# Kernel optimization log

Hardware: AMD Instinct MI355X
Metric: run time of the kernel (lower is better)

The kernel has to match this reference:

```python
import jax, jax.numpy as jnp
import numpy as np

B, S, H, L = 4096, 64, 768, 5
TEMP = 0.07
BN_EPS = 1e-5


def setup_inputs() -> dict:
    key = jax.random.key(0)
    ks = jax.random.split(key, 8)
    seq = jax.random.normal(ks[0], (B, S, H), dtype=jnp.float32)
    labels = jax.random.randint(ks[1], (B,), 0, L)
    s = 1.0 / np.sqrt(H)
    return {
        'sequence_output': seq,
        'cls_gamma': jnp.ones((H,), jnp.float32),
        'cls_beta': jnp.zeros((H,), jnp.float32),
        'cls_W': jax.random.normal(ks[2], (H, H), jnp.float32) * s,
        'cls_b': jax.random.normal(ks[3], (H,), jnp.float32) * 0.01,
        'label_gamma': jnp.ones((H,), jnp.float32),
        'label_beta': jnp.zeros((H,), jnp.float32),
        'label_W': jax.random.normal(ks[4], (H, H), jnp.float32) * s,
        'label_b': jax.random.normal(ks[5], (H,), jnp.float32) * 0.01,
        'labels': labels,
    }


def _batchnorm(x, gamma, beta):
    # training-mode BatchNorm1d: biased batch stats
    m = x.mean(0)
    v = jnp.mean((x - m) ** 2, axis=0)
    return (x - m) * jax.lax.rsqrt(v + BN_EPS) * gamma + beta


def _l2norm(x):
    return x / jnp.sqrt(jnp.sum(x * x, axis=-1, keepdims=True)).clip(1e-12)


def reference(sequence_output, cls_gamma, cls_beta, cls_W, cls_b,
              label_gamma, label_beta, label_W, label_b, labels):
    z = sequence_output[:, 0, :]  # [B,H]; dropout is identity in eval
    # label token spans: 'No relation' -> positions 1:3 (mean), rest single tokens 3..6
    theta = jnp.stack([
        sequence_output[:, 1:3, :].mean(axis=1),
        sequence_output[:, 3, :],
        sequence_output[:, 4, :],
        sequence_output[:, 5, :],
        sequence_output[:, 6, :],
    ], axis=1)  # [B,L,H]
    z_cl, theta_cl = z, theta

    zp = _batchnorm(z, cls_gamma, cls_beta) @ cls_W.T + cls_b  # [B,H]
    tp = _batchnorm(theta.reshape(-1, H), label_gamma, label_beta) @ label_W.T + label_b
    tp = tp.reshape(-1, L, H)  # [B,L,H]
    logits = jnp.einsum('blh,bh->bl', tp, zp)  # [B,L]

    # ---- dual supervised contrastive loss (vectorized over the python loops) ----
    z_norm = _l2norm(z_cl)        # [B,H]
    theta_norm = _l2norm(theta_cl)  # [B,L,H]
    same = labels[:, None] == labels[None, :]          # [B,B]
    eye = jnp.eye(labels.shape[0], dtype=bool)
    pos_mask = (same & ~eye).astype(jnp.float32)       # positives (same label, j != i)
    neg_mask = (~same).astype(jnp.float32)             # negatives (different label)
    has_pos = (same & ~eye).any(axis=1)

    # l_z: anchor z_i vs theta_j[labels_i] (pos) and all theta_j[:] for diff-label j (neg)
    expS = jnp.exp(jnp.einsum('ih,jlh->ijl', z_norm, theta_norm) / TEMP)  # [B,B,L]
    expS_at_lab = jnp.take_along_axis(
        expS, jnp.broadcast_to(labels[:, None, None], expS.shape[:2] + (1,)), axis=2
    )[..., 0]  # expS[i,j,labels[i]] -> [B,B]
    pos_z = jnp.sum(expS_at_lab * pos_mask, axis=1)
    neg_z = jnp.sum(expS.sum(axis=-1) * neg_mask, axis=1)
    l_z = jnp.where(has_pos, -jnp.log(pos_z / (pos_z + neg_z + 1e-8)), 0.0).sum()

    # l_theta: anchor theta_i[labels_i] vs z_j
    anchor_theta = jnp.take_along_axis(theta_norm, labels[:, None, None], axis=1)[:, 0, :]  # [B,H]
    expT = jnp.exp(anchor_theta @ z_norm.T / TEMP)  # [B,B]
    pos_t = jnp.sum(expT * pos_mask, axis=1)
    neg_t = jnp.sum(expT * neg_mask, axis=1)
    l_t = jnp.where(has_pos, -jnp.log(pos_t / (pos_t + neg_t + 1e-8)), 0.0).sum()

    dual_loss = (l_z + l_t) / labels.shape[0]
    return logits, dual_loss
```

## Files before the change

kernel.cpp:

```cpp
#include <hip/hip_runtime.h>
#include <hip/hip_bf16.h>
#include <cstdint>
#include <cstddef>

#define B_N 4096
#define S_N 64
#define H_N 768
#define L_N 5
#define TEMP_INV (1.0f / 0.07f)
#define BN_EPS 1e-5f

typedef __attribute__((ext_vector_type(8))) short short8;
typedef __attribute__((ext_vector_type(4))) float f32x4;

__device__ __forceinline__ void async_copy16(void* lds, const void* g) {
  __builtin_amdgcn_global_load_lds(
      (const __attribute__((address_space(1))) unsigned int*)g,
      (__attribute__((address_space(3))) unsigned int*)lds, 16, 0, 0);
}

__device__ __forceinline__ unsigned short bf16b(float x) {
  __hip_bfloat16 h = __float2bfloat16(x);
  return *reinterpret_cast<unsigned short*>(&h);
}
__device__ __forceinline__ void store_bf16x4(void* p, float4 v) {
  ushort4 o = make_ushort4(bf16b(v.x), bf16b(v.y), bf16b(v.z), bf16b(v.w));
  *reinterpret_cast<ushort4*>(p) = o;
}

__device__ inline float block_reduce_sum256(float v, float* sbuf) {
#pragma unroll
  for (int off = 32; off > 0; off >>= 1) v += __shfl_down(v, off, 64);
  int lane = threadIdx.x & 63;
  int wid = threadIdx.x >> 6;
  __syncthreads();
  if (lane == 0) sbuf[wid] = v;
  __syncthreads();
  float r = 0.f;
  if (threadIdx.x == 0) r = sbuf[0] + sbuf[1] + sbuf[2] + sbuf[3];
  return r;
}

__global__ __launch_bounds__(256) void extract_kernel(
    const float* __restrict__ seq, __hip_bfloat16* __restrict__ zb,
    __hip_bfloat16* __restrict__ tb, float* __restrict__ zn_inv,
    float* __restrict__ thn_inv, float* __restrict__ sum_z,
    float* __restrict__ ssq_z, float* __restrict__ sum_t,
    float* __restrict__ ssq_t) {
  __shared__ float pr[8][6][3];
  int t = threadIdx.x;
  int wv = t >> 6, ln = t & 63;
  bool act = t < 192;
  int c4 = t * 4;
  int b0 = blockIdx.x * 8;
  float zs[4] = {}, zq[4] = {}, ts4[4] = {}, tq4[4] = {};
  for (int r = 0; r < 8; ++r) {
    int b = b0 + r;
    const float* base = seq + (size_t)b * (S_N * H_N);
    float pv[6] = {0.f, 0.f, 0.f, 0.f, 0.f, 0.f};
    if (act) {
      float4 z4 = *(const float4*)(base + c4);
      store_bf16x4(zb + (size_t)b * H_N + c4, z4);
      pv[0] = z4.x * z4.x + z4.y * z4.y + z4.z * z4.z + z4.w * z4.w;
      zs[0] += z4.x; zs[1] += z4.y; zs[2] += z4.z; zs[3] += z4.w;
      zq[0] += z4.x * z4.x; zq[1] += z4.y * z4.y;
      zq[2] += z4.z * z4.z; zq[3] += z4.w * z4.w;
#pragma unroll
      for (int l = 0; l < L_N; ++l) {
        float4 v4;
        if (l == 0) {
          float4 a4 = *(const float4*)(base + H_N + c4);
          float4 b4 = *(const float4*)(base + 2 * H_N + c4);
          v4 = make_float4(0.5f * (a4.x + b4.x), 0.5f * (a4.y + b4.y),
                           0.5f * (a4.z + b4.z), 0.5f * (a4.w + b4.w));
        } else {
          v4 = *(const float4*)(base + (size_t)(l + 2) * H_N + c4);
        }
        store_bf16x4(tb + ((size_t)b * L_N + l) * H_N + c4, v4);
        pv[1 + l] = v4.x * v4.x + v4.y * v4.y + v4.z * v4.z + v4.w * v4.w;
        ts4[0] += v4.x; ts4[1] += v4.y; ts4[2] += v4.z; ts4[3] += v4.w;
        tq4[0] += v4.x * v4.x; tq4[1] += v4.y * v4.y;
        tq4[2] += v4.z * v4.z; tq4[3] += v4.w * v4.w;
      }
    }
#pragma unroll
    for (int v = 0; v < 6; ++v) {
      float x = pv[v];
#pragma unroll
      for (int off = 32; off > 0; off >>= 1) x += __shfl_down(x, off, 64);
      if (ln == 0 && wv < 3) pr[r][v][wv] = x;
    }
  }
  __syncthreads();
  if (t < 48) {
    int r = t / 6, v = t - r * 6;
    float s = pr[r][v][0] + pr[r][v][1] + pr[r][v][2];
    float inv = 1.f / fmaxf(sqrtf(s), 1e-12f);
    int b = b0 + r;
    if (v == 0) zn_inv[b] = inv;
    else thn_inv[b * L_N + (v - 1)] = inv;
  }
  if (act) {
#pragma unroll
    for (int j = 0; j < 4; ++j) {
      atomicAdd(&sum_z[c4 + j], zs[j]);
      atomicAdd(&ssq_z[c4 + j], zq[j]);
      atomicAdd(&sum_t[c4 + j], ts4[j]);
      atomicAdd(&ssq_t[c4 + j], tq4[j]);
    }
  }
}

__global__ void count_kernel(const int* __restrict__ labels, int* __restrict__ cnt) {
  int i = blockIdx.x * 256 + threadIdx.x;
  if (i < B_N) atomicAdd(&cnt[labels[i]], 1);
}

__global__ void finalize_kernel(
    const float* __restrict__ sum_z, const float* __restrict__ ssq_z,
    const float* __restrict__ sum_t, const float* __restrict__ ssq_t,
    const float* __restrict__ g_z, const float* __restrict__ b_z,
    const float* __restrict__ g_t, const float* __restrict__ b_t,
    float* __restrict__ sz_s, float* __restrict__ sz_t,
    float* __restrict__ st_s, float* __restrict__ st_t) {
  int h = blockIdx.x * 256 + threadIdx.x;
  if (h >= H_N) return;
  {
    float m = sum_z[h] * (1.f / B_N);
    float v = ssq_z[h] * (1.f / B_N) - m * m;
    float s = g_z[h] * rsqrtf(v + BN_EPS);
    sz_s[h] = s;
    sz_t[h] = b_z[h] - m * s;
  }
  {
    float m = sum_t[h] * (1.f / (B_N * L_N));
    float v = ssq_t[h] * (1.f / (B_N * L_N)) - m * m;
    float s = g_t[h] * rsqrtf(v + BN_EPS);
    st_s[h] = s;
    st_t[h] = b_t[h] - m * s;
  }
}

__global__ __launch_bounds__(256) void prep_cls_kernel(
    const float* __restrict__ W, const float* __restrict__ szs,
    const float* __restrict__ szt, const float* __restrict__ bias,
    __hip_bfloat16* __restrict__ Wb, float* __restrict__ cprime) {
  __shared__ float sbuf[4];
  int n = blockIdx.x;
  int t = threadIdx.x;
  float dot = 0.f;
  if (t < 192) {
    int c4 = t * 4;
    const float* row = W + (size_t)n * H_N;
    float4 w4 = *(const float4*)(row + c4);
    float4 s4 = *(const float4*)(szs + c4);
    float4 t4 = *(const float4*)(szt + c4);
    store_bf16x4(Wb + (size_t)n * H_N + c4,
                 make_float4(w4.x * s4.x, w4.y * s4.y, w4.z * s4.z, w4.w * s4.w));
    dot = w4.x * t4.x + w4.y * t4.y + w4.z * t4.z + w4.w * t4.w;
  }
  float s = block_reduce_sum256(dot, sbuf);
  if (t == 0) cprime[n] = s + bias[n];
}

__global__ __launch_bounds__(256) void transpose_wl_kernel(
    const float* __restrict__ Wl, __hip_bfloat16* __restrict__ WlT) {
  __shared__ float tile[32][33];
  int t = threadIdx.x;
  int tx = t & 31, ty0 = t >> 5;
  int n0 = blockIdx.x * 32, k0 = blockIdx.y * 32;
#pragma unroll
  for (int p = 0; p < 4; ++p)
    tile[ty0 + p * 8][tx] = Wl[(size_t)(n0 + ty0 + p * 8) * H_N + k0 + tx];
  __syncthreads();
#pragma unroll
  for (int p = 0; p < 4; ++p) {
    unsigned short us = bf16b(tile[tx][ty0 + p * 8]);
    *((unsigned short*)WlT + (size_t)(k0 + ty0 + p * 8) * H_N + n0 + tx) = us;
  }
}

template <bool WRITE_BF16, bool HAS_BIAS>
__global__ __launch_bounds__(256) void gemm128_kernel(
    const __hip_bfloat16* __restrict__ A, const __hip_bfloat16* __restrict__ Bm,
    const float* __restrict__ bias, float* __restrict__ outF,
    __hip_bfloat16* __restrict__ outB) {
  __shared__ __align__(16) __hip_bfloat16 Asm[128 * 32];
  __shared__ __align__(16) __hip_bfloat16 Bsm[128 * 32];
  int tid = threadIdx.x, lane = tid & 63, wid = tid >> 6;
  int wr = wid >> 1, wc = wid & 1;
  int i0 = blockIdx.x * 128, n0 = blockIdx.y * 128;
  int llo = lane & 15, lhi = lane >> 4;
  f32x4 acc[4][4] = {};
  for (int k0 = 0; k0 < H_N; k0 += 32) {
#pragma unroll
    for (int r = 0; r < 2; ++r) {
      int s = r * 256 + wid * 64 + lane;
      int row = s >> 2, kc = (s & 3) * 8;
      size_t go = (size_t)row * H_N + k0 + kc;
      async_copy16((char*)Asm + (size_t)(r * 256 + wid * 64) * 16,
                   A + (size_t)i0 * H_N + go);
      async_copy16((char*)Bsm + (size_t)(r * 256 + wid * 64) * 16,
                   Bm + (size_t)n0 * H_N + go);
    }
    __syncthreads();
    short8 a[4], b[4];
#pragma unroll
    for (int m = 0; m < 4; ++m)
      a[m] = *(const short8*)((const char*)Asm +
                              ((wr * 64 + m * 16 + llo) * 32 + lhi * 8) * 2);
#pragma unroll
    for (int n = 0; n < 4; ++n)
      b[n] = *(const short8*)((const char*)Bsm +
                              ((wc * 64 + n * 16 + llo) * 32 + lhi * 8) * 2);
#pragma unroll
    for (int m = 0; m < 4; ++m)
#pragma unroll
      for (int n = 0; n < 4; ++n)
        acc[m][n] =
            __builtin_amdgcn_mfma_f32_16x16x32_bf16(a[m], b[n], acc[m][n], 0, 0, 0);
    __syncthreads();
  }
#pragma unroll
  for (int n = 0; n < 4; ++n) {
    int col = n0 + wc * 64 + n * 16 + llo;
    float bv = HAS_BIAS ? bias[col] : 0.f;
#pragma unroll
    for (int m = 0; m < 4; ++m) {
#pragma unroll
      for (int r = 0; r < 4; ++r) {
        int row = i0 + wr * 64 + m * 16 + lhi * 4 + r;
        float val = acc[m][n][r] + bv;
        outF[(size_t)row * H_N + col] = val;
        if (WRITE_BF16)
          outB[(size_t)row * H_N + col] = __float2bfloat16(val);
      }
    }
  }
}

__global__ __launch_bounds__(256) void logits_kernel(
    const float* __restrict__ seq, const float* __restrict__ u,
    const float* __restrict__ zp, const float* __restrict__ st_s,
    const float* __restrict__ st_t, const float* __restrict__ label_b,
    float* __restrict__ out) {
  __shared__ float sbuf[4];
  int b = blockIdx.x;
  int t = threadIdx.x;
  bool act = t < 192;
  int c4 = t * 4;
  float4 w4 = make_float4(0.f, 0.f, 0.f, 0.f);
  float apart = 0.f;
  if (act) {
    float4 u4 = *(const float4*)(u + (size_t)b * H_N + c4);
    float4 zp4 = *(const float4*)(zp + (size_t)b * H_N + c4);
    float4 ss4 = *(const float4*)(st_s + c4);
    float4 tt4 = *(const float4*)(st_t + c4);
    float4 lb4 = *(const float4*)(label_b + c4);
    w4 = make_float4(u4.x * ss4.x, u4.y * ss4.y, u4.z * ss4.z, u4.w * ss4.w);
    apart = u4.x * tt4.x + u4.y * tt4.y + u4.z * tt4.z + u4.w * tt4.w +
            zp4.x * lb4.x + zp4.y * lb4.y + zp4.z * lb4.z + zp4.w * lb4.w;
  }
  float alpha = block_reduce_sum256(apart, sbuf);
  const float* base = seq + (size_t)b * (S_N * H_N);
#pragma unroll
  for (int l = 0; l < L_N; ++l) {
    float part = 0.f;
    if (act) {
      float4 v4;
      if (l == 0) {
        float4 a4 = *(const float4*)(base + H_N + c4);
        float4 b4 = *(const float4*)(base + 2 * H_N + c4);
        v4 = make_float4(0.5f * (a4.x + b4.x), 0.5f * (a4.y + b4.y),
                         0.5f * (a4.z + b4.z), 0.5f * (a4.w + b4.w));
      } else {
        v4 = *(const float4*)(base + (size_t)(l + 2) * H_N + c4);
      }
      part = v4.x * w4.x + v4.y * w4.y + v4.z * w4.z + v4.w * w4.w;
    }
    float s = block_reduce_sum256(part, sbuf);
    if (t == 0) out[b * L_N + l] = s + alpha;
  }
}

#define NT_K 24
__global__ __launch_bounds__(512, 1) void sgemm_fused_kernel(
    const __hip_bfloat16* __restrict__ zb, const __hip_bfloat16* __restrict__ tb,
    const float* __restrict__ zn_inv, const float* __restrict__ thn_inv,
    const int* __restrict__ labels, float* __restrict__ pos_z,
    float* __restrict__ neg_z, float* __restrict__ pos_t,
    float* __restrict__ neg_t) {
  __shared__ __align__(128) char ldsbuf[4][32768];

  const int tid = threadIdx.x;
  const int lane = tid & 63, wid = tid >> 6;
  const int llo = lane & 15, lhi = lane >> 4;
  const int wrbase = (wid >> 2) * 128;
  const int wcbase = (wid & 3) * 64;
  const int i0 = blockIdx.x * 256, n0 = blockIdx.y * 256;

  f32x4 acc[8][4] = {};

  auto stageQ = [&](int c, int kt, int q) {
    int s = q * 512 + tid;
    int row = s >> 2;
    int sl = s & 3;
    int lq = sl ^ ((row ^ (row >> 2)) & 3);
    int kofs = kt * 32 + lq * 8;
    int wub = (q * 512 + wid * 64) * 16;
    async_copy16(&ldsbuf[c][0] + wub, zb + (size_t)(i0 + row) * H_N + kofs);
    async_copy16(&ldsbuf[c][16384] + wub, tb + (size_t)(n0 + row) * H_N + kofs);
  };

  stageQ(0, 0, 0); stageQ(0, 0, 1);
  stageQ(1, 1, 0); stageQ(1, 1, 1);
  asm volatile("s_waitcnt vmcnt(4)" ::: "memory");
  __builtin_amdgcn_s_barrier();

  for (int t = 0; t < NT_K; ++t) {
    const char* ldsA = &ldsbuf[t & 3][0];
    const char* ldsB = &ldsbuf[t & 3][16384];
#pragma unroll
    for (int mh = 0; mh < 2; ++mh) {
      short8 a[4], b[4];
#pragma unroll
      for (int m = 0; m < 4; ++m) {
        int row = wrbase + (mh * 4 + m) * 16 + llo;
        a[m] = *(const short8*)(ldsA + row * 64 +
                                ((lhi ^ ((row ^ (row >> 2)) & 3)) * 16));
      }
#pragma unroll
      for (int n = 0; n < 4; ++n) {
        int col = wcbase + n * 16 + llo;
        b[n] = *(const short8*)(ldsB + col * 64 +
                                ((lhi ^ ((col ^ (col >> 2)) & 3)) * 16));
      }
      if (t + 2 < NT_K) stageQ((t + 2) & 3, t + 2, mh);
      __builtin_amdgcn_s_barrier();
      asm volatile("s_waitcnt lgkmcnt(0)" ::: "memory");
      __builtin_amdgcn_sched_barrier(0);
      __builtin_amdgcn_s_setprio(1);
#pragma unroll
      for (int m = 0; m < 4; ++m)
#pragma unroll
        for (int n = 0; n < 4; ++n)
          acc[mh * 4 + m][n] = __builtin_amdgcn_mfma_f32_16x16x32_bf16(
              a[m], b[n], acc[mh * 4 + m][n], 0, 0, 0);
      __builtin_amdgcn_s_setprio(0);
      if (mh == 1) {
        if (t < NT_K - 2)
          asm volatile("s_waitcnt vmcnt(4)" ::: "memory");
        else
          asm volatile("s_waitcnt vmcnt(0)" ::: "memory");
      }
      __builtin_amdgcn_s_barrier();
    }
  }
  __syncthreads();

  float* rpos = (float*)&ldsbuf[0][0];
  float* rneg = rpos + 256;
  float* cpos = rneg + 256;
  float* cneg = cpos + 256;
  float* rnorm = cneg + 256;
  float* cnorm = rnorm + 256;
  int* rowlab = (int*)(cnorm + 256);
  int* colj = rowlab + 256;
  int* coll = colj + 256;
  int* collab = coll + 256;

  if (tid < 256) {
    rowlab[tid] = labels[i0 + tid];
    rnorm[tid] = zn_inv[i0 + tid] * TEMP_INV;
    int c = n0 + tid;
    int j = c / 5;
    colj[tid] = j;
    coll[tid] = c - j * 5;
    collab[tid] = labels[j];
    cnorm[tid] = thn_inv[c];
    rpos[tid] = 0.f; rneg[tid] = 0.f; cpos[tid] = 0.f; cneg[tid] = 0.f;
  }
  __syncthreads();

  int cl[4], jg[4], lv[4], lj[4];
  float cs[4];
#pragma unroll
  for (int ni = 0; ni < 4; ++ni) {
    cl[ni] = wcbase + ni * 16 + llo;
    jg[ni] = colj[cl[ni]];
    lv[ni] = coll[cl[ni]];
    lj[ni] = collab[cl[ni]];
    cs[ni] = cnorm[cl[ni]];
  }
  float cpAcc[4] = {}, cnAcc[4] = {};
#pragma unroll
  for (int mi = 0; mi < 8; ++mi) {
#pragma unroll
    for (int r = 0; r < 4; ++r) {
      int rl = wrbase + mi * 16 + lhi * 4 + r;
      int ig = i0 + rl;
      int li = rowlab[rl];
      float rscale = rnorm[rl];
      float rp = 0.f, rn = 0.f;
#pragma unroll
      for (int ni = 0; ni < 4; ++ni) {
        float e = __expf(acc[mi][ni][r] * rscale * cs[ni]);
        bool same = (li == lj[ni]);
        bool diag = (ig == jg[ni]);
        if (same) {
          if (!diag && lv[ni] == li) { rp += e; cpAcc[ni] += e; }
        } else {
          rn += e;
          if (lv[ni] == lj[ni]) cnAcc[ni] += e;
        }
      }
      if (rp != 0.f) atomicAdd(&rpos[rl], rp);
      if (rn != 0.f) atomicAdd(&rneg[rl], rn);
    }
  }
#pragma unroll
  for (int ni = 0; ni < 4; ++ni) {
    if (cpAcc[ni] != 0.f) atomicAdd(&cpos[cl[ni]], cpAcc[ni]);
    if (cnAcc[ni] != 0.f) atomicAdd(&cneg[cl[ni]], cnAcc[ni]);
  }
  __syncthreads();
  if (tid < 256) {
    float v;
    v = rpos[tid]; if (v != 0.f) atomicAdd(&pos_z[i0 + tid], v);
    v = rneg[tid]; if (v != 0.f) atomicAdd(&neg_z[i0 + tid], v);
    int j = colj[tid];
    v = cpos[tid]; if (v != 0.f) atomicAdd(&pos_t[j], v);
    v = cneg[tid]; if (v != 0.f) atomicAdd(&neg_t[j], v);
  }
}

__global__ __launch_bounds__(256) void loss_kernel(
    const float* __restrict__ pos_z, const float* __restrict__ neg_z,
    const float* __restrict__ pos_t, const float* __restrict__ neg_t,
    const int* __restrict__ labels, const int* __restrict__ cnt,
    float* __restrict__ out_loss) {
  __shared__ float sbuf[4];
  int i = blockIdx.x * 256 + threadIdx.x;
  float term = 0.f;
  int li = labels[i];
  if (cnt[li] > 1) {
    float pz = pos_z[i], nz = neg_z[i];
    float pt = pos_t[i], nt = neg_t[i];
    term = -logf(pz / (pz + nz + 1e-8f)) - logf(pt / (pt + nt + 1e-8f));
  }
  float s = block_reduce_sum256(term, sbuf);
  if (threadIdx.x == 0) atomicAdd(out_loss, s * (1.0f / B_N));
}

extern "C" void kernel_launch(void* const* d_in, const int* in_sizes, int n_in,
                              void* d_out, int out_size, void* d_ws, size_t ws_size,
                              hipStream_t stream) {
  const float* seq = (const float*)d_in[0];
  const float* cls_gamma = (const float*)d_in[1];
  const float* cls_beta = (const float*)d_in[2];
  const float* cls_W = (const float*)d_in[3];
  const float* cls_b = (const float*)d_in[4];
  const float* label_gamma = (const float*)d_in[5];
  const float* label_beta = (const float*)d_in[6];
  const float* label_W = (const float*)d_in[7];
  const float* label_b = (const float*)d_in[8];
  const int* labels = (const int*)d_in[9];
  float* out = (float*)d_out;
  float* ws = (float*)d_ws;

  constexpr size_t OFF_SUMZ = 0;
  constexpr size_t OFF_SSQZ = 768;
  constexpr size_t OFF_SUMT = 1536;
  constexpr size_t OFF_SSQT = 2304;
  constexpr size_t OFF_POSZ = 3072;
  constexpr size_t OFF_NEGZ = 7168;
  constexpr size_t OFF_POST = 11264;
  constexpr size_t OFF_NEGT = 15360;
  constexpr size_t OFF_CNT = 19456;
  constexpr size_t ZERO_FLOATS = 19464;
  constexpr size_t OFF_SZS = 19464;
  constexpr size_t OFF_SZT = 20232;
  constexpr size_t OFF_STS = 21000;
  constexpr size_t OFF_STT = 21768;
  constexpr size_t OFF_ZNI = 22536;
  constexpr size_t OFF_TNI = 26632;
  constexpr size_t OFF_CPRIME = 47112;
  constexpr size_t OFF_ZP = 47880;
  constexpr size_t OFF_U = OFF_ZP + (size_t)B_N * H_N;
  constexpr size_t F32_END = OFF_U + (size_t)B_N * H_N;
  constexpr size_t BYTE_ZB = F32_END * sizeof(float);
  constexpr size_t BYTE_TB = BYTE_ZB + (size_t)B_N * H_N * 2;
  constexpr size_t BYTE_ZPB = BYTE_TB + (size_t)B_N * L_N * H_N * 2;
  constexpr size_t BYTE_WCB = BYTE_ZPB + (size_t)B_N * H_N * 2;
  constexpr size_t BYTE_WLT = BYTE_WCB + (size_t)H_N * H_N * 2;
  constexpr size_t TOTAL_BYTES = BYTE_WLT + (size_t)H_N * H_N * 2;
  if (ws_size < TOTAL_BYTES) return;

  __hip_bfloat16* zb = (__hip_bfloat16*)((char*)d_ws + BYTE_ZB);
  __hip_bfloat16* tb = (__hip_bfloat16*)((char*)d_ws + BYTE_TB);
  __hip_bfloat16* zpb = (__hip_bfloat16*)((char*)d_ws + BYTE_ZPB);
  __hip_bfloat16* wcb = (__hip_bfloat16*)((char*)d_ws + BYTE_WCB);
  __hip_bfloat16* wlt = (__hip_bfloat16*)((char*)d_ws + BYTE_WLT);

  hipMemsetAsync(d_ws, 0, ZERO_FLOATS * sizeof(float), stream);
  hipMemsetAsync((char*)d_out + (size_t)B_N * L_N * sizeof(float), 0, sizeof(float),
                 stream);

  extract_kernel<<<512, 256, 0, stream>>>(seq, zb, tb, ws + OFF_ZNI, ws + OFF_TNI,
                                          ws + OFF_SUMZ, ws + OFF_SSQZ,
                                          ws + OFF_SUMT, ws + OFF_SSQT);
  count_kernel<<<16, 256, 0, stream>>>(labels, (int*)(ws + OFF_CNT));
  finalize_kernel<<<3, 256, 0, stream>>>(
      ws + OFF_SUMZ, ws + OFF_SSQZ, ws + OFF_SUMT, ws + OFF_SSQT, cls_gamma,
      cls_beta, label_gamma, label_beta, ws + OFF_SZS, ws + OFF_SZT, ws + OFF_STS,
      ws + OFF_STT);
  prep_cls_kernel<<<H_N, 256, 0, stream>>>(cls_W, ws + OFF_SZS, ws + OFF_SZT, cls_b,
                                           wcb, ws + OFF_CPRIME);
  transpose_wl_kernel<<<dim3(24, 24), 256, 0, stream>>>(label_W, wlt);
  gemm128_kernel<true, true><<<dim3(32, 6), 256, 0, stream>>>(
      zb, wcb, ws + OFF_CPRIME, ws + OFF_ZP, zpb);
  gemm128_kernel<false, false><<<dim3(32, 6), 256, 0, stream>>>(
      zpb, wlt, nullptr, ws + OFF_U, nullptr);
  logits_kernel<<<B_N, 256, 0, stream>>>(seq, ws + OFF_U, ws + OFF_ZP, ws + OFF_STS,
                                         ws + OFF_STT, label_b, out);
  sgemm_fused_kernel<<<dim3(16, 80), 512, 0, stream>>>(
      zb, tb, ws + OFF_ZNI, ws + OFF_TNI, labels, ws + OFF_POSZ, ws + OFF_NEGZ,
      ws + OFF_POST, ws + OFF_NEGT);
  loss_kernel<<<16, 256, 0, stream>>>(ws + OFF_POSZ, ws + OFF_NEGZ, ws + OFF_POST,
                                      ws + OFF_NEGT, labels,
                                      (const int*)(ws + OFF_CNT),
                                      out + (size_t)B_N * L_N);
}
```

Baseline: 482.2 us.

## Shrink sim GEMM tiles to 128x128 with double buffering and XCD-aware block mapping

Reworks the fused similarity GEMM from 256x256 tiles with 512 threads and a 4-stage LDS ring to 128x128 tiles with 256 threads, a 2-stage LDS buffer, and a new swizzle layout. The grid is flattened to a 1D launch that maps blocks so each XCD works on a contiguous band of rows, aiming for better L2 locality, and launch bounds allow 3 blocks per CU for higher occupancy. In exchange each block reuses loaded data less (lower arithmetic intensity), the pipeline is shallower with a full vmcnt(0) wait every k-step, and more global atomics are issued from the epilogue.

```diff
diff --git a/kernel.cpp b/kernel.cpp
--- a/kernel.cpp
+++ b/kernel.cpp
@@ -284,92 +284,85 @@
 }
 
 #define NT_K 24
-__global__ __launch_bounds__(512, 1) void sgemm_fused_kernel(
+__global__ __launch_bounds__(256, 3) void sgemm_fused_kernel(
     const __hip_bfloat16* __restrict__ zb, const __hip_bfloat16* __restrict__ tb,
     const float* __restrict__ zn_inv, const float* __restrict__ thn_inv,
     const int* __restrict__ labels, float* __restrict__ pos_z,
     float* __restrict__ neg_z, float* __restrict__ pos_t,
     float* __restrict__ neg_t) {
-  __shared__ __align__(128) char ldsbuf[4][32768];
+  __shared__ __align__(128) char ldsbuf[2][16384];
 
   const int tid = threadIdx.x;
   const int lane = tid & 63, wid = tid >> 6;
   const int llo = lane & 15, lhi = lane >> 4;
-  const int wrbase = (wid >> 2) * 128;
-  const int wcbase = (wid & 3) * 64;
-  const int i0 = blockIdx.x * 256, n0 = blockIdx.y * 256;
-
-  f32x4 acc[8][4] = {};
-
-  auto stageQ = [&](int c, int kt, int q) {
-    int s = q * 512 + tid;
-    int row = s >> 2;
-    int sl = s & 3;
-    int lq = sl ^ ((row ^ (row >> 2)) & 3);
-    int kofs = kt * 32 + lq * 8;
-    int wub = (q * 512 + wid * 64) * 16;
-    async_copy16(&ldsbuf[c][0] + wub, zb + (size_t)(i0 + row) * H_N + kofs);
-    async_copy16(&ldsbuf[c][16384] + wub, tb + (size_t)(n0 + row) * H_N + kofs);
+  const int wr = wid >> 1, wc = wid & 1;
+  const int xcd = blockIdx.x & 7;
+  const int s0 = blockIdx.x >> 3;
+  const int i0 = (xcd * 4 + (s0 & 3)) * 128;
+  const int n0 = (s0 >> 2) * 128;
+
+  f32x4 acc[4][4] = {};
+
+  auto stage = [&](int c, int kt) {
+#pragma unroll
+    for (int h = 0; h < 2; ++h) {
+      int s = h * 256 + tid;
+      int R = s >> 3, sp = s & 7;
+      int l = sp ^ (R & 7);
+      int grow = 2 * R + (l >> 2);
+      int gk = kt * 32 + (l & 3) * 8;
+      int wub = (h * 256 + wid * 64) * 16;
+      async_copy16(&ldsbuf[c][0] + wub, zb + (size_t)(i0 + grow) * H_N + gk);
+      async_copy16(&ldsbuf[c][8192] + wub, tb + (size_t)(n0 + grow) * H_N + gk);
+    }
   };
 
-  stageQ(0, 0, 0); stageQ(0, 0, 1);
-  stageQ(1, 1, 0); stageQ(1, 1, 1);
-  asm volatile("s_waitcnt vmcnt(4)" ::: "memory");
+  auto fragOff = [&](int r) {
+    int R = r >> 1;
+    int slot = (r & 1) * 4 + lhi;
+    return R * 128 + ((slot ^ (R & 7)) * 16);
+  };
+
+  stage(0, 0);
+  asm volatile("s_waitcnt vmcnt(0)" ::: "memory");
   __builtin_amdgcn_s_barrier();
 
   for (int t = 0; t < NT_K; ++t) {
-    const char* ldsA = &ldsbuf[t & 3][0];
-    const char* ldsB = &ldsbuf[t & 3][16384];
-#pragma unroll
-    for (int mh = 0; mh < 2; ++mh) {
-      short8 a[4], b[4];
-#pragma unroll
-      for (int m = 0; m < 4; ++m) {
-        int row = wrbase + (mh * 4 + m) * 16 + llo;
-        a[m] = *(const short8*)(ldsA + row * 64 +
-                                ((lhi ^ ((row ^ (row >> 2)) & 3)) * 16));
-      }
-#pragma unroll
-      for (int n = 0; n < 4; ++n) {
-        int col = wcbase + n * 16 + llo;
-        b[n] = *(const short8*)(ldsB + col * 64 +
-                                ((lhi ^ ((col ^ (col >> 2)) & 3)) * 16));
-      }
-      if (t + 2 < NT_K) stageQ((t + 2) & 3, t + 2, mh);
-      __builtin_amdgcn_s_barrier();
-      asm volatile("s_waitcnt lgkmcnt(0)" ::: "memory");
-      __builtin_amdgcn_sched_barrier(0);
-      __builtin_amdgcn_s_setprio(1);
-#pragma unroll
-      for (int m = 0; m < 4; ++m)
-#pragma unroll
-        for (int n = 0; n < 4; ++n)
-          acc[mh * 4 + m][n] = __builtin_amdgcn_mfma_f32_16x16x32_bf16(
-              a[m], b[n], acc[mh * 4 + m][n], 0, 0, 0);
-      __builtin_amdgcn_s_setprio(0);
-      if (mh == 1) {
-        if (t < NT_K - 2)
-          asm volatile("s_waitcnt vmcnt(4)" ::: "memory");
-        else
-          asm volatile("s_waitcnt vmcnt(0)" ::: "memory");
-      }
-      __builtin_amdgcn_s_barrier();
-    }
+    if (t + 1 < NT_K) stage((t + 1) & 1, t + 1);
+    const char* A = &ldsbuf[t & 1][0];
+    const char* B = &ldsbuf[t & 1][8192];
+    short8 a[4], b[4];
+#pragma unroll
+    for (int m = 0; m < 4; ++m) a[m] = *(const short8*)(A + fragOff(wr * 64 + m * 16 + llo));
+#pragma unroll
+    for (int n = 0; n < 4; ++n) b[n] = *(const short8*)(B + fragOff(wc * 64 + n * 16 + llo));
+    asm volatile("s_waitcnt lgkmcnt(0)" ::: "memory");
+    __builtin_amdgcn_sched_barrier(0);
+    __builtin_amdgcn_s_setprio(1);
+#pragma unroll
+    for (int m = 0; m < 4; ++m)
+#pragma unroll
+      for (int n = 0; n < 4; ++n)
+        acc[m][n] =
+            __builtin_amdgcn_mfma_f32_16x16x32_bf16(a[m], b[n], acc[m][n], 0, 0, 0);
+    __builtin_amdgcn_s_setprio(0);
+    asm volatile("s_waitcnt vmcnt(0)" ::: "memory");
+    __builtin_amdgcn_s_barrier();
   }
   __syncthreads();
 
   float* rpos = (float*)&ldsbuf[0][0];
-  float* rneg = rpos + 256;
-  float* cpos = rneg + 256;
-  float* cneg = cpos + 256;
-  float* rnorm = cneg + 256;
-  float* cnorm = rnorm + 256;
-  int* rowlab = (int*)(cnorm + 256);
-  int* colj = rowlab + 256;
-  int* coll = colj + 256;
-  int* collab = coll + 256;
-
-  if (tid < 256) {
+  float* rneg = rpos + 128;
+  float* cpos = rneg + 128;
+  float* cneg = cpos + 128;
+  float* rnorm = cneg + 128;
+  float* cnorm = rnorm + 128;
+  int* rowlab = (int*)(cnorm + 128);
+  int* colj = rowlab + 128;
+  int* coll = colj + 128;
+  int* collab = coll + 128;
+
+  if (tid < 128) {
     rowlab[tid] = labels[i0 + tid];
     rnorm[tid] = zn_inv[i0 + tid] * TEMP_INV;
     int c = n0 + tid;
@@ -386,7 +379,7 @@
   float cs[4];
 #pragma unroll
   for (int ni = 0; ni < 4; ++ni) {
-    cl[ni] = wcbase + ni * 16 + llo;
+    cl[ni] = wc * 64 + ni * 16 + llo;
     jg[ni] = colj[cl[ni]];
     lv[ni] = coll[cl[ni]];
     lj[ni] = collab[cl[ni]];
@@ -394,10 +387,10 @@
   }
   float cpAcc[4] = {}, cnAcc[4] = {};
 #pragma unroll
-  for (int mi = 0; mi < 8; ++mi) {
+  for (int mi = 0; mi < 4; ++mi) {
 #pragma unroll
     for (int r = 0; r < 4; ++r) {
-      int rl = wrbase + mi * 16 + lhi * 4 + r;
+      int rl = wr * 64 + mi * 16 + lhi * 4 + r;
       int ig = i0 + rl;
       int li = rowlab[rl];
       float rscale = rnorm[rl];
@@ -424,7 +417,7 @@
     if (cnAcc[ni] != 0.f) atomicAdd(&cneg[cl[ni]], cnAcc[ni]);
   }
   __syncthreads();
-  if (tid < 256) {
+  if (tid < 128) {
     float v;
     v = rpos[tid]; if (v != 0.f) atomicAdd(&pos_z[i0 + tid], v);
     v = rneg[tid]; if (v != 0.f) atomicAdd(&neg_z[i0 + tid], v);
@@ -523,7 +516,7 @@
       zpb, wlt, nullptr, ws + OFF_U, nullptr);
   logits_kernel<<<B_N, 256, 0, stream>>>(seq, ws + OFF_U, ws + OFF_ZP, ws + OFF_STS,
                                          ws + OFF_STT, label_b, out);
-  sgemm_fused_kernel<<<dim3(16, 80), 512, 0, stream>>>(
+  sgemm_fused_kernel<<<5120, 256, 0, stream>>>(
       zb, tb, ws + OFF_ZNI, ws + OFF_TNI, labels, ws + OFF_POSZ, ws + OFF_NEGZ,
       ws + OFF_POST, ws + OFF_NEGT);
   loss_kernel<<<16, 256, 0, stream>>>(ws + OFF_POSZ, ws + OFF_NEGZ, ws + OFF_POST,
```

After: 461.1 us. 1.05x faster.
